# Optimization experiments

Measured on AMD Instinct MI355X. Metric: run time of the kernel, lower is better.

Reference implementation:

```python
import jax, jax.numpy as jnp
import numpy as np

V, C, D, N_ROUNDS, WIN = 256, 8, 128, 3, 4
B, T = 16, 8192
EPS = 1e-5

def _ln(x, g, b):
    mu = jnp.mean(x, axis=-1, keepdims=True)
    var = jnp.mean((x - mu) ** 2, axis=-1, keepdims=True)
    return (x - mu) * jax.lax.rsqrt(var + EPS) * g + b

def _mlp2(x, w1, b1, w2, b2):
    return jax.nn.gelu(x @ w1 + b1, approximate=False) @ w2 + b2

def setup_inputs() -> dict:
    key = jax.random.key(0)
    ks = iter(jax.random.split(key, 32))
    nrm = lambda shp, s: (jax.random.normal(next(ks), shp, jnp.float32) * s)
    inp = {
        "x": jax.random.randint(next(ks), (B, T), 0, V, dtype=jnp.int32),
        "emb": nrm((V, D), 0.02),
        "pos": nrm((C, D), 0.02),
        # local processor MLP (dim -> 2dim -> dim) + its LayerNorm
        "lw1": nrm((D, 2 * D), 0.05), "lb1": jnp.zeros((2 * D,)),
        "lw2": nrm((2 * D, D), 0.05), "lb2": jnp.zeros((D,)),
        "lln_g": jnp.ones((D,)), "lln_b": jnp.zeros((D,)),
        # chunk pooling
        "pool_w": nrm((D, D), 0.05), "pool_b": jnp.zeros((D,)),
        # message net (2dim -> dim -> dim)
        "msg_w1": nrm((2 * D, D), 0.05), "msg_b1": jnp.zeros((D,)),
        "msg_w2": nrm((D, D), 0.05), "msg_b2": jnp.zeros((D,)),
        # update net (2dim -> dim -> dim)
        "upd_w1": nrm((2 * D, D), 0.05), "upd_b1": jnp.zeros((D,)),
        "upd_w2": nrm((D, D), 0.05), "upd_b2": jnp.zeros((D,)),
        "mln_g": jnp.ones((D,)), "mln_b": jnp.zeros((D,)),
        # broadcast, final LN, head
        "bc_w": nrm((D, D), 0.05), "bc_b": jnp.zeros((D,)),
        "fln_g": jnp.ones((D,)), "fln_b": jnp.zeros((D,)),
        "head_w": nrm((D, V), 0.05),
    }
    return inp

def reference(x, emb, pos, lw1, lb1, lw2, lb2, lln_g, lln_b, pool_w, pool_b,
              msg_w1, msg_b1, msg_w2, msg_b2, upd_w1, upd_b1, upd_w2, upd_b2,
              mln_g, mln_b, bc_w, bc_b, fln_g, fln_b, head_w):
    Bv, Tv = x.shape
    pad = (-Tv) % C
    padded_T = Tv + pad
    n_chunks = padded_T // C
    x_pad = jnp.pad(x, ((0, 0), (0, pad)))
    chunks = x_pad.reshape(Bv, n_chunks, C)

    # local chunk processor (all chunks vectorized; identical per-chunk math)
    h = emb[chunks] + pos[None, None, :, :]              # (B, N, C, D)
    local = h + _mlp2(_ln(h, lln_g, lln_b), lw1, lb1, lw2, lb2)

    summ = local.mean(axis=2) @ pool_w + pool_b          # (B, N, D)

    i = jnp.arange(n_chunks)[:, None]
    d = jnp.arange(WIN + 1)[None, :]
    idx = jnp.clip(i - d, 0, None)
    valid = (i - d >= 0).astype(summ.dtype)
    count = valid.sum(axis=1)                            # (N,)

    hmsg = summ
    for _ in range(N_ROUNDS):
        nbr = hmsg[:, idx]
        self_e = jnp.broadcast_to(hmsg[:, :, None, :], nbr.shape)
        msgs = _mlp2(jnp.concatenate([self_e, nbr], -1), msg_w1, msg_b1, msg_w2, msg_b2)
        agg = (msgs * valid[None, :, :, None]).sum(axis=2) / count[None, :, None]
        upd = _mlp2(jnp.concatenate([hmsg, agg], -1), upd_w1, upd_b1, upd_w2, upd_b2)
        hmsg = _ln(hmsg + upd, mln_g, mln_b)

    bc = hmsg @ bc_w + bc_b                              # (B, N, D)
    combined = (local + bc[:, :, None, :]).reshape(Bv, padded_T, D)[:, :Tv, :]
    logits = _ln(combined, fln_g, fln_b) @ head_w        # (B, T, V)
    return logits
```

## Files before the change

### kernel.cpp

```cpp
#include <hip/hip_runtime.h>

typedef unsigned short u16;
typedef __attribute__((ext_vector_type(8))) __bf16 bf16x8;
typedef __attribute__((ext_vector_type(4))) float floatx4;

#define DEV static __device__ __forceinline__

DEV float lo2f(unsigned v){ return __uint_as_float(v << 16); }
DEV float hi2f(unsigned v){ return __uint_as_float(v & 0xffff0000u); }
DEV u16 f2b(float f){
  unsigned u = __float_as_uint(f);
  return (u16)((u + 0x7fffu + ((u >> 16) & 1u)) >> 16);
}
DEV float geluf(float x){
  float u  = x * 0.70710678118654752440f;
  float au = fabsf(u);
  float t  = __builtin_amdgcn_rcpf(fmaf(0.3275911f, au, 1.0f));
  float p  = t*(0.254829592f + t*(-0.284496736f + t*(1.421413741f +
             t*(-1.453152027f + t*1.061405429f))));
  float e  = __expf(-au*au);
  float E  = fmaf(-p, e, 1.0f);
  float er = copysignf(E, u);
  return 0.5f * x * (1.0f + er);
}

__global__ __launch_bounds__(256) void k_pack(
    const float* __restrict__ lw1, const float* __restrict__ lw2, const float* __restrict__ poolw,
    const float* __restrict__ mw1, const float* __restrict__ mw2, const float* __restrict__ uw1,
    const float* __restrict__ uw2, const float* __restrict__ bcw, const float* __restrict__ headw,
    u16* __restrict__ dst)
{
  int b = blockIdx.x;
  const float* src; int srcN, nbase = 0, off;
  if      (b < 64) {            src = lw1;  srcN = 256; nbase = 0;   off = 0;      }
  else if (b < 128){ b -= 64;   src = lw1;  srcN = 256; nbase = 128; off = 16384;  }
  else if (b < 256){ b -= 128;  src = lw2;  srcN = 128;              off = 32768;  }
  else if (b < 320){ b -= 256;  src = poolw;srcN = 128;              off = 65536;  }
  else if (b < 384){ b -= 320;  src = mw1;  srcN = 128;              off = 81920;  }
  else if (b < 448){ b -= 384;  src = mw1 + 16384; srcN = 128;       off = 98304;  }
  else if (b < 512){ b -= 448;  src = mw2;  srcN = 128;              off = 114688; }
  else if (b < 640){ b -= 512;  src = uw1;  srcN = 128;              off = 131072; }
  else if (b < 704){ b -= 640;  src = uw2;  srcN = 128;              off = 163840; }
  else if (b < 768){ b -= 704;  src = bcw;  srcN = 128;              off = 180224; }
  else if (b < 832){ b -= 768;  src = headw;srcN = 256; nbase = 0;   off = 196608; }
  else             { b -= 832;  src = headw;srcN = 256; nbase = 128; off = 212992; }
  int e = b * 256 + threadIdx.x;
  int j = e & 7, q = (e >> 3) & 3, rest = e >> 5;
  int n = rest & 127, kk = rest >> 7;
  int k = kk * 32 + q * 8 + j;
  dst[off + e] = f2b(src[k * srcN + nbase + n]);
}

DEV void mma8(floatx4* acc, const u16* Arow, int ap, const u16* W, int l15, int q){
  const u16* ar = Arow + l15 * ap + q * 8;
#pragma unroll
  for (int kk = 0; kk < 4; kk++){
    bf16x8 av = *(const bf16x8*)(ar + kk * 32);
#pragma unroll
    for (int nt = 0; nt < 8; nt++){
      bf16x8 bv = *(const bf16x8*)(W + (size_t)((kk * 128 + nt * 16 + l15) * 4 + q) * 8);
      acc[nt] = __builtin_amdgcn_mfma_f32_16x16x32_bf16(av, bv, acc[nt], 0, 0, 0);
    }
  }
}

__global__ __launch_bounds__(256) void k_table(
    const float* __restrict__ emb, const float* __restrict__ pos,
    const u16* __restrict__ lw1p, const float* __restrict__ lb1,
    const u16* __restrict__ lw2p, const float* __restrict__ lb2,
    const float* __restrict__ g, const float* __restrict__ bb,
    u16* __restrict__ table)
{
  __shared__ __align__(16) u16 sA[64][136];
  __shared__ __align__(16) u16 sY[64][136];
  const int tid = threadIdx.x;
  const int m0 = blockIdx.x * 64;
  const int r = tid >> 2, sg = tid & 3;
  {
    const int row = m0 + r, tok = row >> 3, c = row & 7;
    const float4* e4 = (const float4*)(emb + (size_t)tok * 128 + sg * 32);
    const float4* p4 = (const float4*)(pos + c * 128 + sg * 32);
    float h[32];
    float s = 0.f, s2 = 0.f;
#pragma unroll
    for (int i = 0; i < 8; i++){
      float4 ev = e4[i], pv = p4[i];
      float v0 = ev.x + pv.x, v1 = ev.y + pv.y, v2 = ev.z + pv.z, v3 = ev.w + pv.w;
      h[i * 4 + 0] = v0; h[i * 4 + 1] = v1; h[i * 4 + 2] = v2; h[i * 4 + 3] = v3;
      s += v0 + v1 + v2 + v3;
      s2 += v0 * v0 + v1 * v1 + v2 * v2 + v3 * v3;
    }
    s  += __shfl_xor(s, 1, 64);   s  += __shfl_xor(s, 2, 64);
    s2 += __shfl_xor(s2, 1, 64);  s2 += __shfl_xor(s2, 2, 64);
    float mu = s * (1.f / 128.f);
    float rs = rsqrtf(s2 * (1.f / 128.f) - mu * mu + 1e-5f);
#pragma unroll
    for (int i = 0; i < 32; i++){
      int col = sg * 32 + i;
      sA[r][col] = f2b((h[i] - mu) * rs * g[col] + bb[col]);
    }
  }
  __syncthreads();
  const int lane = tid & 63, wv = tid >> 6, l15 = lane & 15, q = lane >> 4;
  floatx4 a2[8];
#pragma unroll
  for (int i = 0; i < 8; i++) a2[i] = (floatx4)(0.0f);
  {
    floatx4 a1[8];
#pragma unroll
    for (int i = 0; i < 8; i++) a1[i] = (floatx4)(0.0f);
    mma8(a1, &sA[wv * 16][0], 136, lw1p, l15, q);
#pragma unroll
    for (int nt = 0; nt < 8; nt++){
      int col = nt * 16 + l15;
      float bval = lb1[col];
#pragma unroll
      for (int rr = 0; rr < 4; rr++)
        sY[wv * 16 + q * 4 + rr][col] = f2b(geluf(a1[nt][rr] + bval));
    }
  }
  __syncthreads();
  mma8(a2, &sY[wv * 16][0], 136, lw2p, l15, q);
  __syncthreads();
  {
    floatx4 a1[8];
#pragma unroll
    for (int i = 0; i < 8; i++) a1[i] = (floatx4)(0.0f);
    mma8(a1, &sA[wv * 16][0], 136, lw1p + 16384, l15, q);
#pragma unroll
    for (int nt = 0; nt < 8; nt++){
      int col = nt * 16 + l15;
      float bval = lb1[128 + col];
#pragma unroll
      for (int rr = 0; rr < 4; rr++)
        sY[wv * 16 + q * 4 + rr][col] = f2b(geluf(a1[nt][rr] + bval));
    }
  }
  __syncthreads();
  mma8(a2, &sY[wv * 16][0], 136, lw2p + 16384, l15, q);
#pragma unroll
  for (int nt = 0; nt < 8; nt++){
    int col = nt * 16 + l15;
    float bval = lb2[col];
#pragma unroll
    for (int rr = 0; rr < 4; rr++){
      int row = wv * 16 + q * 4 + rr;
      int gr = m0 + row, tok = gr >> 3, c = gr & 7;
      float hres = emb[(size_t)tok * 128 + col] + pos[c * 128 + col];
      table[(size_t)gr * 128 + col] = f2b(a2[nt][rr] + bval + hres);
    }
  }
}

__global__ __launch_bounds__(256) void k_summ(
    const int* __restrict__ x, const u16* __restrict__ table, u16* __restrict__ summ)
{
  __shared__ int stok[512];
  const int tid = threadIdx.x;
  const int ch0 = blockIdx.x * 64;
  stok[tid] = x[ch0 * 8 + tid];
  stok[tid + 256] = x[ch0 * 8 + 256 + tid];
  __syncthreads();
  const int lc = tid >> 2, sg = tid & 3;
  float acc[32];
#pragma unroll
  for (int i = 0; i < 32; i++) acc[i] = 0.f;
#pragma unroll
  for (int j = 0; j < 8; j++){
    int row = stok[lc * 8 + j] * 8 + j;
    const uint4* t4 = (const uint4*)(table + (size_t)row * 128 + sg * 32);
#pragma unroll
    for (int i = 0; i < 4; i++){
      uint4 v = t4[i];
      unsigned w[4] = {v.x, v.y, v.z, v.w};
#pragma unroll
      for (int k = 0; k < 4; k++){
        acc[i * 8 + k * 2]     += lo2f(w[k]);
        acc[i * 8 + k * 2 + 1] += hi2f(w[k]);
      }
    }
  }
  unsigned* dst = (unsigned*)(summ + (size_t)(ch0 + lc) * 128 + sg * 32);
#pragma unroll
  for (int i = 0; i < 16; i++)
    dst[i] = (unsigned)f2b(acc[2 * i] * 0.125f) | (((unsigned)f2b(acc[2 * i + 1] * 0.125f)) << 16);
}

DEV void mma_tile4(floatx4* acc, const u16* Arow, int ap, const u16* W,
                   int colbase, int l15, int q){
  const u16* ar = Arow + l15 * ap + q * 8;
#pragma unroll
  for (int kk = 0; kk < 4; kk++){
    bf16x8 av = *(const bf16x8*)(ar + kk * 32);
#pragma unroll
    for (int nt = 0; nt < 4; nt++){
      bf16x8 bv = *(const bf16x8*)(W + (size_t)((kk * 128 + colbase + nt * 16 + l15) * 4 + q) * 8);
      acc[nt] = __builtin_amdgcn_mfma_f32_16x16x32_bf16(av, bv, acc[nt], 0, 0, 0);
    }
  }
}

template<bool GELU>
DEV void store_tile4(const floatx4* acc, const float* bias, u16* Crow, int cp,
                     int colbase, int l15, int q){
#pragma unroll
  for (int nt = 0; nt < 4; nt++){
    int col = colbase + nt * 16 + l15;
    float bval = bias ? bias[col] : 0.f;
#pragma unroll
    for (int rr = 0; rr < 4; rr++){
      float v = acc[nt][rr] + bval;
      if (GELU) v = geluf(v);
      Crow[(q * 4 + rr) * cp + col] = f2b(v);
    }
  }
}

#define PF(P)    do{ const uint4* gs_ = (const uint4*)(P); \
                     pr0 = gs_[tid]; pr1 = gs_[tid + 640]; pr2 = gs_[tid + 1280]; \
                     if (tid < 128) pr3 = gs_[tid + 1920]; }while(0)
#define COMMIT(S) do{ uint4* ss_ = (uint4*)(S); \
                     ss_[tid] = pr0; ss_[tid + 640] = pr1; ss_[tid + 1280] = pr2; \
                     if (tid < 128) ss_[tid + 1920] = pr3; }while(0)

__global__ __launch_bounds__(640, 1) void k_rounds(
    const u16* __restrict__ summB,
    const u16* __restrict__ poolp, const float* __restrict__ poolb,
    const u16* __restrict__ mw1p, const float* __restrict__ mb1,
    const u16* __restrict__ mw2p, const float* __restrict__ mb2,
    const u16* __restrict__ uw1p, const float* __restrict__ ub1,
    const u16* __restrict__ uw2p, const float* __restrict__ ub2,
    const float* __restrict__ mlng, const float* __restrict__ mlnb,
    const u16* __restrict__ bcp, const float* __restrict__ bcb,
    u16* __restrict__ bcB)
{
  __shared__ __align__(16) u16 sH[80][136];
  __shared__ __align__(16) u16 sPQ[80][264];
  __shared__ __align__(16) u16 sS[80][136];
  __shared__ __align__(16) u16 sW0[16384];
  __shared__ __align__(16) u16 sW1[16384];
  const int tid = threadIdx.x;
  const int m0 = blockIdx.x * 64;
  const int halo = (m0 & 1023) ? 12 : 0;
  const int lo = m0 - halo;
  uint4 pr0 = {0,0,0,0}, pr1 = {0,0,0,0}, pr2 = {0,0,0,0}, pr3 = {0,0,0,0};

  PF(poolp);
  {
#pragma unroll
    for (int k = 0; k < 2; k++){
      int idx = tid + k * 640;
      int rr = idx >> 4, c = idx & 15;
      int node = lo + rr; if (node > 16383) node = 16383;
      *(uint4*)&sS[rr][c * 8] = *(const uint4*)(summB + (size_t)node * 128 + c * 8);
    }
  }
  COMMIT(sW0);
  PF(mw1p);
  __syncthreads();

  const int lane = tid & 63, wv = tid >> 6, l15 = lane & 15, q = lane >> 4;
  const int rt = wv >> 1, ch = wv & 1, colbase = ch * 64;
  const int row0 = rt * 16;
  const int d0 = lane * 2;
  const float b1lo = mb1[d0],  b1hi = mb1[d0 + 1];
  const float glo  = mlng[d0], ghi  = mlng[d0 + 1];
  const float blo  = mlnb[d0], bhi  = mlnb[d0 + 1];

  {
    COMMIT(sW1);
    PF(mw1p + 16384);
    floatx4 acc[4];
#pragma unroll
    for (int i = 0; i < 4; i++) acc[i] = (floatx4)(0.0f);
    mma_tile4(acc, &sS[row0][0], 136, sW0, colbase, l15, q);
    store_tile4<false>(acc, poolb, &sH[row0][0], 136, colbase, l15, q);
  }
  __syncthreads();

  for (int rnd = 0; rnd < 3; rnd++){
    {
      COMMIT(sW0);
      PF(mw2p);
      floatx4 acc[4];
#pragma unroll
      for (int i = 0; i < 4; i++) acc[i] = (floatx4)(0.0f);
      mma_tile4(acc, &sH[row0][0], 136, sW1, colbase, l15, q);
      store_tile4<false>(acc, nullptr, &sPQ[row0][0], 264, colbase, l15, q);
    }
    __syncthreads();
    {
      COMMIT(sW1);
      PF(uw1p);
      floatx4 acc[4];
#pragma unroll
      for (int i = 0; i < 4; i++) acc[i] = (floatx4)(0.0f);
      mma_tile4(acc, &sH[row0][0], 136, sW0, colbase, l15, q);
      store_tile4<false>(acc, nullptr, &sPQ[row0][128], 264, colbase, l15, q);
    }
    __syncthreads();
    {
      for (int it = 0; it < 8; it++){
        int rr = wv * 8 + it;
        int i = (lo + rr) & 1023;
        int nd = (i + 1 < 5) ? i + 1 : 5;
        int ndc = (nd < rr + 1) ? nd : rr + 1;
        unsigned pv = *(const unsigned*)&sPQ[rr][d0];
        float p0 = lo2f(pv) + b1lo, p1 = hi2f(pv) + b1hi;
        float a0 = 0.f, a1 = 0.f;
        for (int d = 0; d < ndc; d++){
          unsigned qv = *(const unsigned*)&sPQ[rr - d][128 + d0];
          a0 += geluf(p0 + lo2f(qv));
          a1 += geluf(p1 + hi2f(qv));
        }
        float inv = 1.f / (float)nd;
        unsigned pack = (unsigned)f2b(a0 * inv) | (((unsigned)f2b(a1 * inv)) << 16);
        *(unsigned*)&sS[rr][d0] = pack;
      }
    }
    __syncthreads();
    {
      COMMIT(sW0);
      PF(uw1p + 16384);
      floatx4 acc[4];
#pragma unroll
      for (int i = 0; i < 4; i++) acc[i] = (floatx4)(0.0f);
      mma_tile4(acc, &sS[row0][0], 136, sW1, colbase, l15, q);
      store_tile4<false>(acc, mb2, &sPQ[row0][0], 264, colbase, l15, q);
    }
    __syncthreads();
    floatx4 acc2[4];
    {
      COMMIT(sW1);
      PF(uw2p);
#pragma unroll
      for (int i = 0; i < 4; i++) acc2[i] = (floatx4)(0.0f);
      mma_tile4(acc2, &sH[row0][0], 136, sW0, colbase, l15, q);
    }
    __syncthreads();
    {
      COMMIT(sW0);
      PF(rnd < 2 ? mw1p : bcp);
      mma_tile4(acc2, &sPQ[row0][0], 264, sW1, colbase, l15, q);
      store_tile4<true>(acc2, ub1, &sS[row0][0], 136, colbase, l15, q);
    }
    __syncthreads();
    {
      COMMIT(sW1);
      if (rnd < 2) PF(mw1p + 16384);
      floatx4 acc[4];
#pragma unroll
      for (int i = 0; i < 4; i++) acc[i] = (floatx4)(0.0f);
      mma_tile4(acc, &sS[row0][0], 136, sW0, colbase, l15, q);
      store_tile4<false>(acc, ub2, &sPQ[row0][128], 264, colbase, l15, q);
    }
    __syncthreads();
    {
      for (int it = 0; it < 8; it++){
        int rr = wv * 8 + it;
        unsigned hv = *(const unsigned*)&sH[rr][d0];
        unsigned uv = *(const unsigned*)&sPQ[rr][128 + d0];
        float x0 = lo2f(hv) + lo2f(uv);
        float x1 = hi2f(hv) + hi2f(uv);
        float s = x0 + x1, s2 = x0 * x0 + x1 * x1;
#pragma unroll
        for (int off = 32; off; off >>= 1){
          s  += __shfl_xor(s, off, 64);
          s2 += __shfl_xor(s2, off, 64);
        }
        float mu = s * (1.f / 128.f);
        float rs = rsqrtf(s2 * (1.f / 128.f) - mu * mu + 1e-5f);
        float y0 = (x0 - mu) * rs * glo + blo;
        float y1 = (x1 - mu) * rs * ghi + bhi;
        unsigned pack = (unsigned)f2b(y0) | (((unsigned)f2b(y1)) << 16);
        *(unsigned*)&sH[rr][d0] = pack;
      }
    }
    __syncthreads();
  }
  {
    floatx4 acc[4];
#pragma unroll
    for (int i = 0; i < 4; i++) acc[i] = (floatx4)(0.0f);
    mma_tile4(acc, &sH[row0][0], 136, sW1, colbase, l15, q);
#pragma unroll
    for (int nt = 0; nt < 4; nt++){
      int col = colbase + nt * 16 + l15;
      float bval = bcb[col];
#pragma unroll
      for (int rr = 0; rr < 4; rr++){
        int row = row0 + q * 4 + rr;
        if (row >= halo && row < halo + 64){
          int node = lo + row;
          bcB[(size_t)node * 128 + col] = f2b(acc[nt][rr] + bval);
        }
      }
    }
  }
}

#define PF512(P)  do{ const uint4* gs_ = (const uint4*)(P); \
                      pr0 = gs_[tid]; pr1 = gs_[tid + 512]; \
                      pr2 = gs_[tid + 1024]; pr3 = gs_[tid + 1536]; }while(0)
#define CM512(S)  do{ uint4* ss_ = (uint4*)(S); \
                      ss_[tid] = pr0; ss_[tid + 512] = pr1; \
                      ss_[tid + 1024] = pr2; ss_[tid + 1536] = pr3; }while(0)

__global__ __launch_bounds__(512, 1) void k_head(
    const int* __restrict__ x, const u16* __restrict__ table,
    const u16* __restrict__ bcB,
    const float* __restrict__ g, const float* __restrict__ bb,
    const u16* __restrict__ headp, float* __restrict__ out)
{
  __shared__ __align__(16) u16 sA[128][136];
  __shared__ __align__(16) u16 sW0[16384], sW1[16384];
  const int tid = threadIdx.x;
  const int m0 = blockIdx.x * 128;
  uint4 pr0, pr1, pr2, pr3;
  PF512(headp);
  const int r = tid >> 2, sg = tid & 3;
  {
    const int gr = m0 + r;
    const int trow = x[gr] * 8 + (gr & 7);
    const uint4* l4 = (const uint4*)(table + (size_t)trow * 128 + sg * 32);
    const uint4* c4 = (const uint4*)(bcB + (size_t)(gr >> 3) * 128 + sg * 32);
    float h[32];
    float s = 0.f, s2 = 0.f;
#pragma unroll
    for (int i = 0; i < 4; i++){
      uint4 lv = l4[i], cv = c4[i];
      unsigned lw[4] = {lv.x, lv.y, lv.z, lv.w}, cw[4] = {cv.x, cv.y, cv.z, cv.w};
#pragma unroll
      for (int j = 0; j < 4; j++){
        float v0 = lo2f(lw[j]) + lo2f(cw[j]);
        float v1 = hi2f(lw[j]) + hi2f(cw[j]);
        h[i * 8 + j * 2] = v0; h[i * 8 + j * 2 + 1] = v1;
        s += v0 + v1; s2 += v0 * v0 + v1 * v1;
      }
    }
    s  += __shfl_xor(s, 1, 64);   s  += __shfl_xor(s, 2, 64);
    s2 += __shfl_xor(s2, 1, 64);  s2 += __shfl_xor(s2, 2, 64);
    float mu = s * (1.f / 128.f);
    float rs = rsqrtf(s2 * (1.f / 128.f) - mu * mu + 1e-5f);
#pragma unroll
    for (int i = 0; i < 32; i++){
      int col = sg * 32 + i;
      sA[r][col] = f2b((h[i] - mu) * rs * g[col] + bb[col]);
    }
  }
  CM512(sW0);
  PF512(headp + 16384);
  __syncthreads();
  const int lane = tid & 63, wv = tid >> 6, l15 = lane & 15, q = lane >> 4;
  {
    floatx4 acc[8];
#pragma unroll
    for (int i = 0; i < 8; i++) acc[i] = (floatx4)(0.0f);
    mma8(acc, &sA[wv * 16][0], 136, sW0, l15, q);
    CM512(sW1);
#pragma unroll
    for (int nt = 0; nt < 8; nt++){
      int col = nt * 16 + l15;
#pragma unroll
      for (int rr = 0; rr < 4; rr++){
        int row = wv * 16 + q * 4 + rr;
        out[(size_t)(m0 + row) * 256 + col] = acc[nt][rr];
      }
    }
  }
  __syncthreads();
  {
    floatx4 acc[8];
#pragma unroll
    for (int i = 0; i < 8; i++) acc[i] = (floatx4)(0.0f);
    mma8(acc, &sA[wv * 16][0], 136, sW1, l15, q);
#pragma unroll
    for (int nt = 0; nt < 8; nt++){
      int col = 128 + nt * 16 + l15;
#pragma unroll
      for (int rr = 0; rr < 4; rr++){
        int row = wv * 16 + q * 4 + rr;
        out[(size_t)(m0 + row) * 256 + col] = acc[nt][rr];
      }
    }
  }
}


extern "C" void kernel_launch(void* const* d_in, const int* in_sizes, int n_in,
                              void* d_out, int out_size, void* d_ws, size_t ws_size,
                              hipStream_t stream)
{
  const int*   x     = (const int*)d_in[0];
  const float* emb   = (const float*)d_in[1];
  const float* pos   = (const float*)d_in[2];
  const float* lw1   = (const float*)d_in[3];
  const float* lb1   = (const float*)d_in[4];
  const float* lw2   = (const float*)d_in[5];
  const float* lb2   = (const float*)d_in[6];
  const float* llng  = (const float*)d_in[7];
  const float* llnb  = (const float*)d_in[8];
  const float* poolw = (const float*)d_in[9];
  const float* poolb = (const float*)d_in[10];
  const float* mw1   = (const float*)d_in[11];
  const float* mb1   = (const float*)d_in[12];
  const float* mw2   = (const float*)d_in[13];
  const float* mb2   = (const float*)d_in[14];
  const float* uw1   = (const float*)d_in[15];
  const float* ub1   = (const float*)d_in[16];
  const float* uw2   = (const float*)d_in[17];
  const float* ub2   = (const float*)d_in[18];
  const float* mlng  = (const float*)d_in[19];
  const float* mlnb  = (const float*)d_in[20];
  const float* bcw   = (const float*)d_in[21];
  const float* bcb   = (const float*)d_in[22];
  const float* flng  = (const float*)d_in[23];
  const float* flnb  = (const float*)d_in[24];
  const float* headw = (const float*)d_in[25];

  char* ws = (char*)d_ws;
  u16* wpack = (u16*)ws;
  u16* lw1p  = wpack;
  u16* lw2p  = wpack + 32768;
  u16* poolp = wpack + 65536;
  u16* mw1p  = wpack + 81920;
  u16* mw2p  = wpack + 114688;
  u16* uw1p  = wpack + 131072;
  u16* uw2p  = wpack + 163840;
  u16* bcp   = wpack + 180224;
  u16* headp = wpack + 196608;
  u16* table = (u16*)(ws + 524288);
  u16* summB = (u16*)(ws + 1048576);
  u16* bcB   = (u16*)(ws + 5242880);

  k_pack<<<896, 256, 0, stream>>>(lw1, lw2, poolw, mw1, mw2, uw1, uw2, bcw, headw, wpack);
  k_table<<<32, 256, 0, stream>>>(emb, pos, lw1p, lb1, lw2p, lb2, llng, llnb, table);
  k_summ<<<256, 256, 0, stream>>>(x, table, summB);
  k_rounds<<<256, 640, 0, stream>>>(summB, poolp, poolb, mw1p, mb1, mw2p, mb2,
                                    uw1p, ub1, uw2p, ub2, mlng, mlnb, bcp, bcb, bcB);
  k_head<<<1024, 512, 0, stream>>>(x, table, bcB, flng, flnb, headp, (float*)d_out);
}
```

Measured before the change: 312.9 us.

## Read most round weights directly from global, keep msg_w1 resident; halve head LDS

In the message-passing kernel, the rotating double-buffered LDS weight staging (prefetch/commit per stage) is replaced. The full msg_w1 (both halves) is now kept resident in LDS, and the two P/Q products are merged into one wider mma8 pass per wave. Pool, msg_w2, upd_w1, upd_w2 and bc weights are passed straight to mma_tile4 as global pointers, and two update-MLP stages are fused to cut barriers. The head kernel uses a single LDS weight buffer with an extra barrier so two blocks can fit per CU. The tradeoff is global or L2 weight reads inside the MMA loops, and whether mma_tile4 accepts global pointers efficiently is unclear.

```diff
diff --git a/kernel.cpp b/kernel.cpp
--- a/kernel.cpp
+++ b/kernel.cpp
@@ -216,13 +216,6 @@
   }
 }
 
-#define PF(P)    do{ const uint4* gs_ = (const uint4*)(P); \
-                     pr0 = gs_[tid]; pr1 = gs_[tid + 640]; pr2 = gs_[tid + 1280]; \
-                     if (tid < 128) pr3 = gs_[tid + 1920]; }while(0)
-#define COMMIT(S) do{ uint4* ss_ = (uint4*)(S); \
-                     ss_[tid] = pr0; ss_[tid + 640] = pr1; ss_[tid + 1280] = pr2; \
-                     if (tid < 128) ss_[tid + 1920] = pr3; }while(0)
-
 __global__ __launch_bounds__(640, 1) void k_rounds(
     const u16* __restrict__ summB,
     const u16* __restrict__ poolp, const float* __restrict__ poolb,
@@ -237,16 +230,16 @@
   __shared__ __align__(16) u16 sH[80][136];
   __shared__ __align__(16) u16 sPQ[80][264];
   __shared__ __align__(16) u16 sS[80][136];
-  __shared__ __align__(16) u16 sW0[16384];
-  __shared__ __align__(16) u16 sW1[16384];
+  __shared__ __align__(16) u16 sW[32768];
   const int tid = threadIdx.x;
   const int m0 = blockIdx.x * 64;
   const int halo = (m0 & 1023) ? 12 : 0;
   const int lo = m0 - halo;
-  uint4 pr0 = {0,0,0,0}, pr1 = {0,0,0,0}, pr2 = {0,0,0,0}, pr3 = {0,0,0,0};
-
-  PF(poolp);
-  {
+
+  {
+    const uint4* gs = (const uint4*)mw1p;
+    uint4* ss = (uint4*)sW;
+    for (int i = tid; i < 4096; i += 640) ss[i] = gs[i];
 #pragma unroll
     for (int k = 0; k < 2; k++){
       int idx = tid + k * 640;
@@ -255,8 +248,6 @@
       *(uint4*)&sS[rr][c * 8] = *(const uint4*)(summB + (size_t)node * 128 + c * 8);
     }
   }
-  COMMIT(sW0);
-  PF(mw1p);
   __syncthreads();
 
   const int lane = tid & 63, wv = tid >> 6, l15 = lane & 15, q = lane >> 4;
@@ -268,35 +259,27 @@
   const float blo  = mlnb[d0], bhi  = mlnb[d0 + 1];
 
   {
-    COMMIT(sW1);
-    PF(mw1p + 16384);
     floatx4 acc[4];
 #pragma unroll
     for (int i = 0; i < 4; i++) acc[i] = (floatx4)(0.0f);
-    mma_tile4(acc, &sS[row0][0], 136, sW0, colbase, l15, q);
+    mma_tile4(acc, &sS[row0][0], 136, poolp, colbase, l15, q);
     store_tile4<false>(acc, poolb, &sH[row0][0], 136, colbase, l15, q);
   }
   __syncthreads();
 
   for (int rnd = 0; rnd < 3; rnd++){
     {
-      COMMIT(sW0);
-      PF(mw2p);
-      floatx4 acc[4];
-#pragma unroll
-      for (int i = 0; i < 4; i++) acc[i] = (floatx4)(0.0f);
-      mma_tile4(acc, &sH[row0][0], 136, sW1, colbase, l15, q);
-      store_tile4<false>(acc, nullptr, &sPQ[row0][0], 264, colbase, l15, q);
-    }
-    __syncthreads();
-    {
-      COMMIT(sW1);
-      PF(uw1p);
-      floatx4 acc[4];
-#pragma unroll
-      for (int i = 0; i < 4; i++) acc[i] = (floatx4)(0.0f);
-      mma_tile4(acc, &sH[row0][0], 136, sW0, colbase, l15, q);
-      store_tile4<false>(acc, nullptr, &sPQ[row0][128], 264, colbase, l15, q);
+      floatx4 acc[8];
+#pragma unroll
+      for (int i = 0; i < 8; i++) acc[i] = (floatx4)(0.0f);
+      mma8(acc, &sH[row0][0], 136, sW + ch * 16384, l15, q);
+#pragma unroll
+      for (int nt = 0; nt < 8; nt++){
+        int col = ch * 128 + nt * 16 + l15;
+#pragma unroll
+        for (int rr = 0; rr < 4; rr++)
+          sPQ[row0 + q * 4 + rr][col] = f2b(acc[nt][rr]);
+      }
     }
     __syncthreads();
     {
@@ -320,38 +303,27 @@
     }
     __syncthreads();
     {
-      COMMIT(sW0);
-      PF(uw1p + 16384);
       floatx4 acc[4];
 #pragma unroll
       for (int i = 0; i < 4; i++) acc[i] = (floatx4)(0.0f);
-      mma_tile4(acc, &sS[row0][0], 136, sW1, colbase, l15, q);
+      mma_tile4(acc, &sS[row0][0], 136, mw2p, colbase, l15, q);
       store_tile4<false>(acc, mb2, &sPQ[row0][0], 264, colbase, l15, q);
-    }
-    __syncthreads();
-    floatx4 acc2[4];
-    {
-      COMMIT(sW1);
-      PF(uw2p);
-#pragma unroll
-      for (int i = 0; i < 4; i++) acc2[i] = (floatx4)(0.0f);
-      mma_tile4(acc2, &sH[row0][0], 136, sW0, colbase, l15, q);
     }
     __syncthreads();
     {
-      COMMIT(sW0);
-      PF(rnd < 2 ? mw1p : bcp);
-      mma_tile4(acc2, &sPQ[row0][0], 264, sW1, colbase, l15, q);
-      store_tile4<true>(acc2, ub1, &sS[row0][0], 136, colbase, l15, q);
+      floatx4 acc[4];
+#pragma unroll
+      for (int i = 0; i < 4; i++) acc[i] = (floatx4)(0.0f);
+      mma_tile4(acc, &sH[row0][0], 136, uw1p, colbase, l15, q);
+      mma_tile4(acc, &sPQ[row0][0], 264, uw1p + 16384, colbase, l15, q);
+      store_tile4<true>(acc, ub1, &sS[row0][0], 136, colbase, l15, q);
     }
     __syncthreads();
     {
-      COMMIT(sW1);
-      if (rnd < 2) PF(mw1p + 16384);
       floatx4 acc[4];
 #pragma unroll
       for (int i = 0; i < 4; i++) acc[i] = (floatx4)(0.0f);
-      mma_tile4(acc, &sS[row0][0], 136, sW0, colbase, l15, q);
+      mma_tile4(acc, &sS[row0][0], 136, uw2p, colbase, l15, q);
       store_tile4<false>(acc, ub2, &sPQ[row0][128], 264, colbase, l15, q);
     }
     __syncthreads();
@@ -382,7 +354,7 @@
     floatx4 acc[4];
 #pragma unroll
     for (int i = 0; i < 4; i++) acc[i] = (floatx4)(0.0f);
-    mma_tile4(acc, &sH[row0][0], 136, sW1, colbase, l15, q);
+    mma_tile4(acc, &sH[row0][0], 136, bcp, colbase, l15, q);
 #pragma unroll
     for (int nt = 0; nt < 4; nt++){
       int col = colbase + nt * 16 + l15;
@@ -399,26 +371,22 @@
   }
 }
 
-#define PF512(P)  do{ const uint4* gs_ = (const uint4*)(P); \
-                      pr0 = gs_[tid]; pr1 = gs_[tid + 512]; \
-                      pr2 = gs_[tid + 1024]; pr3 = gs_[tid + 1536]; }while(0)
-#define CM512(S)  do{ uint4* ss_ = (uint4*)(S); \
-                      ss_[tid] = pr0; ss_[tid + 512] = pr1; \
-                      ss_[tid + 1024] = pr2; ss_[tid + 1536] = pr3; }while(0)
-
-__global__ __launch_bounds__(512, 1) void k_head(
+__global__ __launch_bounds__(512, 2) void k_head(
     const int* __restrict__ x, const u16* __restrict__ table,
     const u16* __restrict__ bcB,
     const float* __restrict__ g, const float* __restrict__ bb,
     const u16* __restrict__ headp, float* __restrict__ out)
 {
   __shared__ __align__(16) u16 sA[128][136];
-  __shared__ __align__(16) u16 sW0[16384], sW1[16384];
+  __shared__ __align__(16) u16 sW[16384];
   const int tid = threadIdx.x;
   const int m0 = blockIdx.x * 128;
-  uint4 pr0, pr1, pr2, pr3;
-  PF512(headp);
   const int r = tid >> 2, sg = tid & 3;
+  uint4 pa0, pa1, pa2, pa3;
+  {
+    const uint4* gs = (const uint4*)headp;
+    pa0 = gs[tid]; pa1 = gs[tid + 512]; pa2 = gs[tid + 1024]; pa3 = gs[tid + 1536];
+  }
   {
     const int gr = m0 + r;
     const int trow = x[gr] * 8 + (gr & 7);
@@ -448,16 +416,22 @@
       sA[r][col] = f2b((h[i] - mu) * rs * g[col] + bb[col]);
     }
   }
-  CM512(sW0);
-  PF512(headp + 16384);
+  {
+    uint4* ss = (uint4*)sW;
+    ss[tid] = pa0; ss[tid + 512] = pa1; ss[tid + 1024] = pa2; ss[tid + 1536] = pa3;
+  }
+  uint4 pb0, pb1, pb2, pb3;
+  {
+    const uint4* gs = (const uint4*)(headp + 16384);
+    pb0 = gs[tid]; pb1 = gs[tid + 512]; pb2 = gs[tid + 1024]; pb3 = gs[tid + 1536];
+  }
   __syncthreads();
   const int lane = tid & 63, wv = tid >> 6, l15 = lane & 15, q = lane >> 4;
   {
     floatx4 acc[8];
 #pragma unroll
     for (int i = 0; i < 8; i++) acc[i] = (floatx4)(0.0f);
-    mma8(acc, &sA[wv * 16][0], 136, sW0, l15, q);
-    CM512(sW1);
+    mma8(acc, &sA[wv * 16][0], 136, sW, l15, q);
 #pragma unroll
     for (int nt = 0; nt < 8; nt++){
       int col = nt * 16 + l15;
@@ -470,10 +444,15 @@
   }
   __syncthreads();
   {
+    uint4* ss = (uint4*)sW;
+    ss[tid] = pb0; ss[tid + 512] = pb1; ss[tid + 1024] = pb2; ss[tid + 1536] = pb3;
+  }
+  __syncthreads();
+  {
     floatx4 acc[8];
 #pragma unroll
     for (int i = 0; i < 8; i++) acc[i] = (floatx4)(0.0f);
-    mma8(acc, &sA[wv * 16][0], 136, sW1, l15, q);
+    mma8(acc, &sA[wv * 16][0], 136, sW, l15, q);
 #pragma unroll
     for (int nt = 0; nt < 8; nt++){
       int col = 128 + nt * 16 + l15;
```

New measurement: 376.6 us. +20.4%, slower.
